# Optimization experiments

Measured on AMD Instinct MI355X. Metric: run time of the kernel, lower is better.

Reference implementation:

```python
import jax, jax.numpy as jnp
import numpy as np

B, L, D_IN, D_OUT = 4, 256, 256, 256


def setup_inputs() -> dict:
    key = jax.random.key(0)
    k1, k2, k3, k4, k5 = jax.random.split(key, 5)
    text = jax.random.normal(k1, (B, L, D_IN), dtype=jnp.float32)
    adj = jax.random.uniform(k2, (B, L, L), dtype=jnp.float32)
    dep_embed = jax.random.normal(k3, (B, L, L, D_IN), dtype=jnp.float32)
    # nn.Linear default init scale ~ 1/sqrt(fan_in); use small random weights
    W = jax.random.normal(k4, (D_OUT, D_IN), dtype=jnp.float32) / jnp.sqrt(D_IN).astype(jnp.float32)
    b = jax.random.normal(k5, (D_OUT,), dtype=jnp.float32) * 0.01
    return {"text": text, "adj": adj, "dep_embed": dep_embed, "W": W, "b": b}


def reference(text, adj, dep_embed, W, b):
    # val_sum[b,i,j,d] = text[b,i,d] + dep_embed[b,i,j,d]   -> [B,L,L,D]
    val_sum = text[:, :, None, :] + dep_embed
    # hidden = Linear(val_sum): [B,L,L,D_out]
    hidden = jnp.einsum('bijd,od->bijo', val_sum, W) + b
    # output[b,i,o] = sum_j hidden[b,j,i,o] * adj[b,i,j]  (transpose(1,2) then adj-mask then sum over dim 2)
    output = jnp.einsum('bjio,bij->bio', hidden, adj)
    return output
```

## Files before the change

kernel.cpp:

```cpp
#include <hip/hip_runtime.h>


#define LL 256
#define DD 256
#define D4 64

typedef float float4n __attribute__((ext_vector_type(4)));

__global__ __launch_bounds__(256, 8) void tgc_phase1(
    const float* __restrict__ text,
    const float* __restrict__ adj,
    const float* __restrict__ dep,
    float4* __restrict__ spS)
{
    const int bid = blockIdx.x;
    const int jh  = bid & 1;
    const int bi  = bid >> 1;
    const int b   = bi >> 8;
    const int i   = bi & 255;
    const int t   = threadIdx.x;
    const int g   = t >> 6;
    const int l   = t & 63;

    __shared__ float  adjs[128];
    __shared__ float4 red[4][64];

    if (t < 128) adjs[t] = adj[bi * LL + jh * 128 + t];
    __syncthreads();

    const float4n* __restrict__ dep4 = (const float4n*)dep;
    const float4*  __restrict__ text4 = (const float4*)text;

    float4 acc = make_float4(0.f, 0.f, 0.f, 0.f);

    {
        const float4n* dp = dep4 + (((size_t)(b * LL + jh * 128 + g) * LL + i) * D4 + l);
        const size_t   JS = (size_t)4 * LL * D4;
        #pragma unroll 4
        for (int jj = 0; jj < 32; ++jj) {
            const float   a = adjs[(jj << 2) + g];
            const float4n d = __builtin_nontemporal_load(dp);
            acc.x += a * d.x;
            acc.y += a * d.y;
            acc.z += a * d.z;
            acc.w += a * d.w;
            dp += JS;
        }
    }
    {
        const float4* tp = text4 + ((size_t)(b * LL + jh * 128 + g) * D4 + l);
        const size_t  TS = (size_t)4 * D4;
        #pragma unroll 4
        for (int jj = 0; jj < 32; ++jj) {
            const float  a  = adjs[(jj << 2) + g];
            const float4 tv = *tp;
            acc.x += a * tv.x;
            acc.y += a * tv.y;
            acc.z += a * tv.z;
            acc.w += a * tv.w;
            tp += TS;
        }
    }

    red[g][l] = acc;
    __syncthreads();
    if (g == 0) {
        const float4 r0 = red[0][l], r1 = red[1][l], r2 = red[2][l], r3 = red[3][l];
        spS[(size_t)bid * 64 + l] = make_float4(r0.x + r1.x + r2.x + r3.x,
                                                r0.y + r1.y + r2.y + r3.y,
                                                r0.z + r1.z + r2.z + r3.z,
                                                r0.w + r1.w + r2.w + r3.w);
    }
}

__global__ __launch_bounds__(256) void tgc_phase2(
    const float* __restrict__ adj,
    const float4* __restrict__ spS,
    const float* __restrict__ W,
    const float* __restrict__ bias,
    float* __restrict__ out)
{
    const int bi = blockIdx.x;
    const int t  = threadIdx.x;
    const int w  = t >> 6;
    const int l  = t & 63;

    __shared__ float4 sfin[64];
    __shared__ float  ared[4];

    float av = adj[bi * LL + t];
    #pragma unroll
    for (int off = 32; off > 0; off >>= 1) av += __shfl_down(av, off);
    if (l == 0) ared[w] = av;

    if (w == 0) {
        const float4 s0 = spS[(size_t)(bi * 2)     * 64 + l];
        const float4 s1 = spS[(size_t)(bi * 2 + 1) * 64 + l];
        sfin[l] = make_float4(s0.x + s1.x, s0.y + s1.y, s0.z + s1.z, s0.w + s1.w);
    }
    __syncthreads();

    const float A = ared[0] + ared[1] + ared[2] + ared[3];

    const float4* W4 = (const float4*)W;
    float oacc = 0.f;
    #pragma unroll 8
    for (int d4 = 0; d4 < D4; ++d4) {
        const float4 s  = sfin[d4];
        const float4 wv = W4[t * D4 + d4];
        oacc += s.x * wv.x + s.y * wv.y + s.z * wv.z + s.w * wv.w;
    }
    out[bi * DD + t] = oacc + A * bias[t];
}

extern "C" void kernel_launch(void* const* d_in, const int* in_sizes, int n_in,
                              void* d_out, int out_size, void* d_ws, size_t ws_size,
                              hipStream_t stream) {
    const float* text = (const float*)d_in[0];
    const float* adj  = (const float*)d_in[1];
    const float* dep  = (const float*)d_in[2];
    const float* W    = (const float*)d_in[3];
    const float* bias = (const float*)d_in[4];
    float* out = (float*)d_out;
    float4* spS = (float4*)d_ws;

    tgc_phase1<<<dim3(2048), dim3(256), 0, stream>>>(text, adj, dep, spS);
    tgc_phase2<<<dim3(1024), dim3(256), 0, stream>>>(adj, spS, W, bias, out);
}
```

Baseline: 378.3 us.

## Fuse adjacency-weighted reduction and linear projection into a single kernel

Merges the two kernels into one. Each block now handles the whole j range for a given (b,i) instead of half of it, and then applies the W projection and bias from shared memory. This drops the workspace round trip and the second launch. In exchange, the block count halves from 2048 to 1024, which reduces parallelism for the memory-bound dep_embed stream, and the launch-bounds occupancy hint drops from 8 to 4.

```diff
diff --git a/kernel.cpp b/kernel.cpp
--- a/kernel.cpp
+++ b/kernel.cpp
@@ -7,37 +7,40 @@
 
 typedef float float4n __attribute__((ext_vector_type(4)));
 
-__global__ __launch_bounds__(256, 8) void tgc_phase1(
+__global__ __launch_bounds__(256, 4) void tgc_fused(
     const float* __restrict__ text,
     const float* __restrict__ adj,
     const float* __restrict__ dep,
-    float4* __restrict__ spS)
+    const float* __restrict__ W,
+    const float* __restrict__ bias,
+    float* __restrict__ out)
 {
-    const int bid = blockIdx.x;
-    const int jh  = bid & 1;
-    const int bi  = bid >> 1;
-    const int b   = bi >> 8;
-    const int i   = bi & 255;
-    const int t   = threadIdx.x;
-    const int g   = t >> 6;
-    const int l   = t & 63;
+    const int bi = blockIdx.x;
+    const int b  = bi >> 8;
+    const int i  = bi & 255;
+    const int t  = threadIdx.x;
+    const int g  = t >> 6;
+    const int l  = t & 63;
 
-    __shared__ float  adjs[128];
+    __shared__ float  adjs[LL];
     __shared__ float4 red[4][64];
+    __shared__ float4 sfin[64];
+    __shared__ float  ared[4];
 
-    if (t < 128) adjs[t] = adj[bi * LL + jh * 128 + t];
+    const float av = adj[bi * LL + t];
+    adjs[t] = av;
     __syncthreads();
 
-    const float4n* __restrict__ dep4 = (const float4n*)dep;
+    const float4n* __restrict__ dep4  = (const float4n*)dep;
     const float4*  __restrict__ text4 = (const float4*)text;
 
     float4 acc = make_float4(0.f, 0.f, 0.f, 0.f);
 
     {
-        const float4n* dp = dep4 + (((size_t)(b * LL + jh * 128 + g) * LL + i) * D4 + l);
+        const float4n* dp = dep4 + (((size_t)(b * LL + g) * LL + i) * D4 + l);
         const size_t   JS = (size_t)4 * LL * D4;
         #pragma unroll 4
-        for (int jj = 0; jj < 32; ++jj) {
+        for (int jj = 0; jj < 64; ++jj) {
             const float   a = adjs[(jj << 2) + g];
             const float4n d = __builtin_nontemporal_load(dp);
             acc.x += a * d.x;
@@ -48,10 +51,10 @@
         }
     }
     {
-        const float4* tp = text4 + ((size_t)(b * LL + jh * 128 + g) * D4 + l);
+        const float4* tp = text4 + ((size_t)(b * LL + g) * D4 + l);
         const size_t  TS = (size_t)4 * D4;
         #pragma unroll 4
-        for (int jj = 0; jj < 32; ++jj) {
+        for (int jj = 0; jj < 64; ++jj) {
             const float  a  = adjs[(jj << 2) + g];
             const float4 tv = *tp;
             acc.x += a * tv.x;
@@ -62,41 +65,19 @@
         }
     }
 
+    float avs = av;
+    #pragma unroll
+    for (int off = 32; off > 0; off >>= 1) avs += __shfl_down(avs, off);
+    if (l == 0) ared[g] = avs;
+
     red[g][l] = acc;
     __syncthreads();
     if (g == 0) {
         const float4 r0 = red[0][l], r1 = red[1][l], r2 = red[2][l], r3 = red[3][l];
-        spS[(size_t)bid * 64 + l] = make_float4(r0.x + r1.x + r2.x + r3.x,
-                                                r0.y + r1.y + r2.y + r3.y,
-                                                r0.z + r1.z + r2.z + r3.z,
-                                                r0.w + r1.w + r2.w + r3.w);
-    }
-}
-
-__global__ __launch_bounds__(256) void tgc_phase2(
-    const float* __restrict__ adj,
-    const float4* __restrict__ spS,
-    const float* __restrict__ W,
-    const float* __restrict__ bias,
-    float* __restrict__ out)
-{
-    const int bi = blockIdx.x;
-    const int t  = threadIdx.x;
-    const int w  = t >> 6;
-    const int l  = t & 63;
-
-    __shared__ float4 sfin[64];
-    __shared__ float  ared[4];
-
-    float av = adj[bi * LL + t];
-    #pragma unroll
-    for (int off = 32; off > 0; off >>= 1) av += __shfl_down(av, off);
-    if (l == 0) ared[w] = av;
-
-    if (w == 0) {
-        const float4 s0 = spS[(size_t)(bi * 2)     * 64 + l];
-        const float4 s1 = spS[(size_t)(bi * 2 + 1) * 64 + l];
-        sfin[l] = make_float4(s0.x + s1.x, s0.y + s1.y, s0.z + s1.z, s0.w + s1.w);
+        sfin[l] = make_float4(r0.x + r1.x + r2.x + r3.x,
+                              r0.y + r1.y + r2.y + r3.y,
+                              r0.z + r1.z + r2.z + r3.z,
+                              r0.w + r1.w + r2.w + r3.w);
     }
     __syncthreads();
 
@@ -122,8 +103,6 @@
     const float* W    = (const float*)d_in[3];
     const float* bias = (const float*)d_in[4];
     float* out = (float*)d_out;
-    float4* spS = (float4*)d_ws;
 
-    tgc_phase1<<<dim3(2048), dim3(256), 0, stream>>>(text, adj, dep, spS);
-    tgc_phase2<<<dim3(1024), dim3(256), 0, stream>>>(adj, spS, W, bias, out);
+    tgc_fused<<<dim3(1024), dim3(256), 0, stream>>>(text, adj, dep, W, bias, out);
 }
```

Result: no change. 376.0 us (-0.6%).
